# Optimization experiments

Hardware: AMD Instinct MI355X
Metric: run time of the kernel (lower is better)

Reference implementation:

```python
import jax, jax.numpy as jnp
import numpy as np
import math

NEG_INF = -1e29
B, L, H = 16, 1024, 512
D = 2 * H          # feature dim of s and q
GELU_C = math.sqrt(2.0 / math.pi)


def gelu(x):
    return 0.5 * x * (1.0 + jnp.tanh(GELU_C * (x + 0.044715 * x ** 3)))


def mask_softmax(W, m1, m2):
    # joint mask: [B, len1, 1] * [B, 1, len2]
    m = (m1[:, :, None] * m2[:, None, :]).astype(W.dtype)
    return jax.nn.softmax(W + (1.0 - m) * NEG_INF, axis=-1)


def heuristic(x, y, w_r, b_r, w_g, b_g):
    inp = jnp.concatenate([x, y, x * y, x - y], axis=-1)  # [B, L, 8H]
    r = gelu(inp @ w_r.T + b_r)                           # [B, L, 2H]
    g = jax.nn.sigmoid(inp @ w_g.T + b_g)
    return g * r + (1.0 - g) * x


def setup_inputs() -> dict:
    key = jax.random.key(0)
    k = jax.random.split(key, 6)
    s = jax.random.normal(k[0], (B, L, D), jnp.float32)
    q = jax.random.normal(k[1], (B, L, D), jnp.float32)
    s_mask = jnp.ones((B, L), jnp.int32)
    q_mask = jnp.ones((B, L), jnp.int32)
    fan_in = 8 * H
    lim = 1.0 / np.sqrt(fan_in)
    w_r = jax.random.uniform(k[2], (2 * H, fan_in), jnp.float32, -lim, lim)
    b_r = jax.random.uniform(k[3], (2 * H,), jnp.float32, -lim, lim)
    w_g = jax.random.uniform(k[4], (2 * H, fan_in), jnp.float32, -lim, lim)
    b_g = jax.random.uniform(k[5], (2 * H,), jnp.float32, -lim, lim)
    return {"s": s, "q": q, "w_r": w_r, "b_r": b_r, "w_g": w_g, "b_g": b_g,
            "s_mask": s_mask, "q_mask": q_mask}


def reference(s, q, w_r, b_r, w_g, b_g, s_mask, q_mask):
    a = jnp.einsum('bsd,btd->bst', s, q)                  # [B, Ls, Lq]
    b = mask_softmax(a, s_mask, q_mask) @ q               # [B, Ls, D]
    c = mask_softmax(a.swapaxes(-1, -2), q_mask, s_mask) @ s  # [B, Lq, D]
    s_tilde = heuristic(s, b, w_r, b_r, w_g, b_g)
    q_tilde = heuristic(q, c, w_r, b_r, w_g, b_g)
    return (s_tilde, q_tilde)
```

## Files before the change

kernel.cpp:

```cpp
#include <hip/hip_runtime.h>
#include <hip/hip_bf16.h>
#include <math.h>

#define DEVI static __device__ __forceinline__

typedef unsigned short u16;
typedef unsigned int u32;
typedef __bf16 bf16_t;
typedef bf16_t bf16x8 __attribute__((ext_vector_type(8)));
typedef float f32x4 __attribute__((ext_vector_type(4)));

static constexpr int Bb = 16;
static constexpr int L  = 1024;
static constexpr int D  = 1024;
static constexpr int KH = 4096;

DEVI u16 f2bf(float f) {
  union { float f; u32 u; } v; v.f = f;
  u32 r = v.u + 0x7FFFu + ((v.u >> 16) & 1u);
  return (u16)(r >> 16);
}

DEVI float bf2f(u16 b) {
  union { u32 u; float f; } v; v.u = ((u32)b) << 16;
  return v.f;
}

DEVI void gload16(const void* g, void* l) {
  __builtin_amdgcn_global_load_lds((const __attribute__((address_space(1))) u32*)g,
                                   (__attribute__((address_space(3))) u32*)l,
                                   16, 0, 0);
}

DEVI int swz(int row, int col) { return col ^ ((row & 7) << 3); }

__global__ void k_cast_bf16(const float* __restrict__ in, u16* __restrict__ out, int n4) {
  int i = blockIdx.x * blockDim.x + threadIdx.x;
  int stride = gridDim.x * blockDim.x;
  for (; i < n4; i += stride) {
    float4 v = ((const float4*)in)[i];
    ushort4 o;
    o.x = f2bf(v.x); o.y = f2bf(v.y); o.z = f2bf(v.z); o.w = f2bf(v.w);
    ((ushort4*)out)[i] = o;
  }
}

__global__ void k_cast_split(const float* __restrict__ in, u16* __restrict__ hi,
                             u16* __restrict__ lo, int n4) {
  int i = blockIdx.x * blockDim.x + threadIdx.x;
  int stride = gridDim.x * blockDim.x;
  for (; i < n4; i += stride) {
    float4 v = ((const float4*)in)[i];
    ushort4 h, l;
    h.x = f2bf(v.x); h.y = f2bf(v.y); h.z = f2bf(v.z); h.w = f2bf(v.w);
    l.x = f2bf(v.x - bf2f(h.x));
    l.y = f2bf(v.y - bf2f(h.y));
    l.z = f2bf(v.z - bf2f(h.z));
    l.w = f2bf(v.w - bf2f(h.w));
    ((ushort4*)hi)[i] = h;
    ((ushort4*)lo)[i] = l;
  }
}

__global__ void k_feat(const u16* __restrict__ x, const u16* __restrict__ y,
                       u16* __restrict__ xy, u16* __restrict__ xmy, int n8) {
  int i = blockIdx.x * blockDim.x + threadIdx.x;
  int stride = gridDim.x * blockDim.x;
  for (; i < n8; i += stride) {
    bf16x8 xv = ((const bf16x8*)x)[i];
    bf16x8 yv = ((const bf16x8*)y)[i];
    bf16x8 p, d;
    #pragma unroll
    for (int j = 0; j < 8; ++j) {
      float xf = (float)xv[j], yf = (float)yv[j];
      p[j] = (bf16_t)(xf * yf);
      d[j] = (bf16_t)(xf - yf);
    }
    ((bf16x8*)xy)[i] = p;
    ((bf16x8*)xmy)[i] = d;
  }
}

__global__ __launch_bounds__(256)
void k_transpose_bf16(const float* __restrict__ in, u16* __restrict__ out) {
  __shared__ float tile[32][33];
  int b = blockIdx.z;
  int d0 = blockIdx.x * 32;
  int l0 = blockIdx.y * 32;
  const float* ip = in + (size_t)b * L * D;
  u16* op = out + (size_t)b * L * D;
  int tx = threadIdx.x, ty = threadIdx.y;
  #pragma unroll
  for (int j = 0; j < 4; ++j)
    tile[ty + 8 * j][tx] = ip[(size_t)(l0 + ty + 8 * j) * D + d0 + tx];
  __syncthreads();
  #pragma unroll
  for (int j = 0; j < 4; ++j)
    op[(size_t)(d0 + ty + 8 * j) * L + l0 + tx] = f2bf(tile[tx][ty + 8 * j]);
}

template<int OUT_BF16>
__global__ __launch_bounds__(256, 4)
void k_gemm_nt(const u16* __restrict__ A, const u16* __restrict__ Bm, void* __restrict__ Cv,
               int K, int ldc, size_t sA, size_t sB, size_t sC, int tilesN)
{
  __shared__ __align__(16) u16 As[128 * 64];
  __shared__ __align__(16) u16 Bs[128 * 64];
  const int bx = blockIdx.x;
  const int tm = bx / tilesN, tn = bx % tilesN;
  const int b = blockIdx.y;
  const u16* Ap = A + (size_t)b * sA + (size_t)tm * 128 * K;
  const u16* Bp = Bm + (size_t)b * sB + (size_t)tn * 128 * K;
  const int tid = threadIdx.x;
  const int lane = tid & 63, wv = tid >> 6;
  const int wm = wv >> 1, wn = wv & 1;
  const int srow = tid >> 3;
  const int scol = (tid & 7) * 8;
  const int scolswz = swz(srow, scol);
  f32x4 acc[4][4] = {};
  for (int k0 = 0; k0 < K; k0 += 64) {
    #pragma unroll
    for (int i = 0; i < 4; ++i) {
      int row = i * 32 + srow;
      gload16(Ap + (size_t)row * K + k0 + scolswz, &As[row * 64 + scol]);
    }
    #pragma unroll
    for (int i = 0; i < 4; ++i) {
      int row = i * 32 + srow;
      gload16(Bp + (size_t)row * K + k0 + scolswz, &Bs[row * 64 + scol]);
    }
    __syncthreads();
    const int hi8 = (lane >> 4) * 8;
    #pragma unroll
    for (int kk = 0; kk < 64; kk += 32) {
      bf16x8 af[4], bfv[4];
      #pragma unroll
      for (int m = 0; m < 4; ++m) {
        int rr = wm * 64 + m * 16 + (lane & 15);
        af[m] = *(const bf16x8*)&As[rr * 64 + swz(rr, kk + hi8)];
      }
      #pragma unroll
      for (int n = 0; n < 4; ++n) {
        int rr = wn * 64 + n * 16 + (lane & 15);
        bfv[n] = *(const bf16x8*)&Bs[rr * 64 + swz(rr, kk + hi8)];
      }
      #pragma unroll
      for (int m = 0; m < 4; ++m)
        #pragma unroll
        for (int n = 0; n < 4; ++n)
          acc[m][n] = __builtin_amdgcn_mfma_f32_16x16x32_bf16(af[m], bfv[n], acc[m][n], 0, 0, 0);
    }
    __syncthreads();
  }
  const int rb = tm * 128 + wm * 64 + ((lane >> 4) << 2);
  const int cb = tn * 128 + wn * 64 + (lane & 15);
  #pragma unroll
  for (int m = 0; m < 4; ++m)
    #pragma unroll
    for (int n = 0; n < 4; ++n)
      #pragma unroll
      for (int j = 0; j < 4; ++j) {
        int r = rb + m * 16 + j, c = cb + n * 16;
        if (OUT_BF16)
          ((u16*)Cv)[(size_t)b * sC + (size_t)r * ldc + c] = f2bf(acc[m][n][j]);
        else
          ((float*)Cv)[(size_t)b * sC + (size_t)r * ldc + c] = acc[m][n][j];
      }
}

__global__ __launch_bounds__(256, 2)
void k_gemm_nt_split(const u16* __restrict__ Ah, const u16* __restrict__ Al,
                     const u16* __restrict__ Bh, const u16* __restrict__ Bl,
                     float* __restrict__ C, int K, int ldc, size_t sAB, size_t sC, int tilesN)
{
  __shared__ __align__(16) u16 Ahs[128 * 64];
  __shared__ __align__(16) u16 Als[128 * 64];
  __shared__ __align__(16) u16 Bhs[128 * 64];
  __shared__ __align__(16) u16 Bls[128 * 64];
  const int bx = blockIdx.x;
  const int tm = bx / tilesN, tn = bx % tilesN;
  const int b = blockIdx.y;
  const size_t aoff = (size_t)b * sAB + (size_t)tm * 128 * K;
  const size_t boff = (size_t)b * sAB + (size_t)tn * 128 * K;
  const int tid = threadIdx.x;
  const int lane = tid & 63, wv = tid >> 6;
  const int wm = wv >> 1, wn = wv & 1;
  const int srow = tid >> 3;
  const int scol = (tid & 7) * 8;
  const int scolswz = swz(srow, scol);
  f32x4 acc[4][4] = {};
  for (int k0 = 0; k0 < K; k0 += 64) {
    #pragma unroll
    for (int i = 0; i < 4; ++i) {
      int row = i * 32 + srow;
      size_t ga = aoff + (size_t)row * K + k0 + scolswz;
      size_t gb = boff + (size_t)row * K + k0 + scolswz;
      int ls = row * 64 + scol;
      gload16(Ah + ga, &Ahs[ls]);
      gload16(Al + ga, &Als[ls]);
      gload16(Bh + gb, &Bhs[ls]);
      gload16(Bl + gb, &Bls[ls]);
    }
    __syncthreads();
    const int hi8 = (lane >> 4) * 8;
    #pragma unroll
    for (int kk = 0; kk < 64; kk += 32) {
      bf16x8 ah[4], al[4], bh[4], bl[4];
      #pragma unroll
      for (int m = 0; m < 4; ++m) {
        int rr = wm * 64 + m * 16 + (lane & 15);
        int off = rr * 64 + swz(rr, kk + hi8);
        ah[m] = *(const bf16x8*)&Ahs[off];
        al[m] = *(const bf16x8*)&Als[off];
      }
      #pragma unroll
      for (int n = 0; n < 4; ++n) {
        int rr = wn * 64 + n * 16 + (lane & 15);
        int off = rr * 64 + swz(rr, kk + hi8);
        bh[n] = *(const bf16x8*)&Bhs[off];
        bl[n] = *(const bf16x8*)&Bls[off];
      }
      #pragma unroll
      for (int m = 0; m < 4; ++m)
        #pragma unroll
        for (int n = 0; n < 4; ++n) {
          acc[m][n] = __builtin_amdgcn_mfma_f32_16x16x32_bf16(ah[m], bh[n], acc[m][n], 0, 0, 0);
          acc[m][n] = __builtin_amdgcn_mfma_f32_16x16x32_bf16(ah[m], bl[n], acc[m][n], 0, 0, 0);
          acc[m][n] = __builtin_amdgcn_mfma_f32_16x16x32_bf16(al[m], bh[n], acc[m][n], 0, 0, 0);
        }
    }
    __syncthreads();
  }
  const int rb = tm * 128 + wm * 64 + ((lane >> 4) << 2);
  const int cb = tn * 128 + wn * 64 + (lane & 15);
  #pragma unroll
  for (int m = 0; m < 4; ++m)
    #pragma unroll
    for (int n = 0; n < 4; ++n)
      #pragma unroll
      for (int j = 0; j < 4; ++j) {
        int r = rb + m * 16 + j, c = cb + n * 16;
        C[(size_t)b * sC + (size_t)r * ldc + c] = acc[m][n][j];
      }
}

__global__ __launch_bounds__(256)
void k_row_softmax(const float* __restrict__ a, u16* __restrict__ P,
                   const int* __restrict__ m1, const int* __restrict__ m2)
{
  const int row = blockIdx.x, b = blockIdx.y;
  const float* ar = a + ((size_t)b * L + row) * L;
  const int tid = threadIdx.x, lane = tid & 63, wv = tid >> 6;
  __shared__ float redm[4], reds[4];
  float4 v = ((const float4*)ar)[tid];
  int4 mv = ((const int4*)(m2 + (size_t)b * L))[tid];
  const int mr = m1[(size_t)b * L + row];
  float x0 = v.x + (float)(1 - mr * mv.x) * (-1e29f);
  float x1 = v.y + (float)(1 - mr * mv.y) * (-1e29f);
  float x2 = v.z + (float)(1 - mr * mv.z) * (-1e29f);
  float x3 = v.w + (float)(1 - mr * mv.w) * (-1e29f);
  float mx = fmaxf(fmaxf(x0, x1), fmaxf(x2, x3));
  #pragma unroll
  for (int o = 32; o > 0; o >>= 1) mx = fmaxf(mx, __shfl_xor(mx, o));
  if (lane == 0) redm[wv] = mx;
  __syncthreads();
  mx = fmaxf(fmaxf(redm[0], redm[1]), fmaxf(redm[2], redm[3]));
  float e0 = __expf(x0 - mx), e1 = __expf(x1 - mx), e2 = __expf(x2 - mx), e3 = __expf(x3 - mx);
  float s4 = e0 + e1 + e2 + e3;
  #pragma unroll
  for (int o = 32; o > 0; o >>= 1) s4 += __shfl_xor(s4, o);
  if (lane == 0) reds[wv] = s4;
  __syncthreads();
  float inv = 1.0f / (reds[0] + reds[1] + reds[2] + reds[3]);
  ushort4 o;
  o.x = f2bf(e0 * inv); o.y = f2bf(e1 * inv); o.z = f2bf(e2 * inv); o.w = f2bf(e3 * inv);
  ((ushort4*)(P + ((size_t)b * L + row) * L))[tid] = o;
}

__global__ __launch_bounds__(256)
void k_col_softmax(const float* __restrict__ a, u16* __restrict__ P,
                   const int* __restrict__ mrow, const int* __restrict__ mcol)
{
  __shared__ float mred[4][64], lred[4][64];
  __shared__ float Mc[64], Li[64];
  __shared__ u16 T[64][68];
  const int b = blockIdx.y;
  const int c0 = blockIdx.x * 64;
  const int tid = threadIdx.x;
  const int cl = tid & 63;
  const int qr = tid >> 6;
  const int c = c0 + cl;
  const float* ab = a + (size_t)b * L * L;
  const int mc = mcol[(size_t)b * L + c];
  const int* msk = mrow + (size_t)b * L;
  float m = -3.0e38f, l = 0.0f;
  for (int r = qr * 256; r < qr * 256 + 256; ++r) {
    float x = ab[(size_t)r * L + c] + (float)(1 - mc * msk[r]) * (-1e29f);
    float mn = fmaxf(m, x);
    l = l * __expf(m - mn) + __expf(x - mn);
    m = mn;
  }
  mred[qr][cl] = m; lred[qr][cl] = l;
  __syncthreads();
  if (tid < 64) {
    float M = fmaxf(fmaxf(mred[0][tid], mred[1][tid]), fmaxf(mred[2][tid], mred[3][tid]));
    float Lt = lred[0][tid] * __expf(mred[0][tid] - M) + lred[1][tid] * __expf(mred[1][tid] - M)
             + lred[2][tid] * __expf(mred[2][tid] - M) + lred[3][tid] * __expf(mred[3][tid] - M);
    Mc[tid] = M; Li[tid] = 1.0f / Lt;
  }
  __syncthreads();
  const float M = Mc[cl], Linv = Li[cl];
  u16* Pb = P + (size_t)b * L * L;
  const int tl = tid >> 2, sc = (tid & 3) * 16;
  for (int ch = 0; ch < 16; ++ch) {
    #pragma unroll
    for (int rs = 0; rs < 16; ++rs) {
      int r = ch * 64 + qr * 16 + rs;
      float x = ab[(size_t)r * L + c] + (float)(1 - mc * msk[r]) * (-1e29f);
      T[cl][qr * 16 + rs] = f2bf(__expf(x - M) * Linv);
    }
    __syncthreads();
    ushort4* d4 = (ushort4*)(Pb + (size_t)(c0 + tl) * L + ch * 64 + sc);
    #pragma unroll
    for (int jj = 0; jj < 4; ++jj) {
      ushort4 v;
      v.x = T[tl][sc + jj * 4 + 0]; v.y = T[tl][sc + jj * 4 + 1];
      v.z = T[tl][sc + jj * 4 + 2]; v.w = T[tl][sc + jj * 4 + 3];
      d4[jj] = v;
    }
    __syncthreads();
  }
}

__global__ __launch_bounds__(512, 2)
void k_heur3(const u16* __restrict__ X, const u16* __restrict__ Y,
             const u16* __restrict__ XY, const u16* __restrict__ XMY,
             const u16* __restrict__ Wr, const u16* __restrict__ Wg,
             const float* __restrict__ br, const float* __restrict__ bg,
             const float* __restrict__ Xf, float* __restrict__ out)
{
  __shared__ __align__(16) u16 As[2][256 * 64];
  __shared__ __align__(16) u16 Wrs[2][128 * 64];
  __shared__ __align__(16) u16 Wgs[2][128 * 64];
  const int bx = blockIdx.x;
  const int xcd = bx & 7, li = bx >> 3;
  const int tn = li & 7, tm = xcd * 8 + (li >> 3);
  const size_t rowBase = (size_t)tm * 256;
  const int tid = threadIdx.x, lane = tid & 63;
  const int wv = tid >> 6;
  const int wm = wv >> 1, wn = wv & 1;
  const int srow = tid >> 3;
  const int scol = (tid & 7) * 8;
  const int scolswz = swz(srow, scol);
  f32x4 accR[4][4] = {}, accG[4][4] = {};

  auto stage = [&](int t, int buf) {
    const int fa = t >> 4;
    const u16* ap = (fa == 0) ? X : (fa == 1) ? Y : (fa == 2) ? XY : XMY;
    const int kcol = (t & 15) * 64;
    #pragma unroll
    for (int i = 0; i < 4; ++i) {
      int row = i * 64 + srow;
      gload16(ap + (rowBase + row) * (size_t)D + kcol + scolswz, &As[buf][row * 64 + scol]);
    }
    const size_t wcol = (size_t)t * 64;
    #pragma unroll
    for (int i = 0; i < 2; ++i) {
      int row = i * 64 + srow;
      size_t woff = ((size_t)tn * 128 + row) * (size_t)KH + wcol + scolswz;
      gload16(Wr + woff, &Wrs[buf][row * 64 + scol]);
      gload16(Wg + woff, &Wgs[buf][row * 64 + scol]);
    }
  };

  stage(0, 0);
  __syncthreads();

  for (int t = 0; t < 64; ++t) {
    const int cur = t & 1;
    if (t < 63) stage(t + 1, cur ^ 1);

    const int hi8 = (lane >> 4) * 8;
    #pragma unroll
    for (int kk = 0; kk < 64; kk += 32) {
      bf16x8 af[4];
      #pragma unroll
      for (int m = 0; m < 4; ++m) {
        int rr = wm * 64 + m * 16 + (lane & 15);
        af[m] = *(const bf16x8*)&As[cur][rr * 64 + swz(rr, kk + hi8)];
      }
      #pragma unroll
      for (int n = 0; n < 4; ++n) {
        int rr = wn * 64 + n * 16 + (lane & 15);
        int off = rr * 64 + swz(rr, kk + hi8);
        bf16x8 bR = *(const bf16x8*)&Wrs[cur][off];
        bf16x8 bG = *(const bf16x8*)&Wgs[cur][off];
        #pragma unroll
        for (int m = 0; m < 4; ++m) {
          accR[m][n] = __builtin_amdgcn_mfma_f32_16x16x32_bf16(af[m], bR, accR[m][n], 0, 0, 0);
          accG[m][n] = __builtin_amdgcn_mfma_f32_16x16x32_bf16(af[m], bG, accG[m][n], 0, 0, 0);
        }
      }
    }
    __syncthreads();
  }

  const int rb = wm * 64 + ((lane >> 4) << 2);
  const int cb = tn * 128 + wn * 64 + (lane & 15);
  #pragma unroll
  for (int m = 0; m < 4; ++m)
    #pragma unroll
    for (int n = 0; n < 4; ++n)
      #pragma unroll
      for (int j = 0; j < 4; ++j) {
        size_t row = rowBase + rb + m * 16 + j;
        int col = cb + n * 16;
        float r = accR[m][n][j] + br[col];
        float g = accG[m][n][j] + bg[col];
        float th = tanhf(0.79788456080286535588f * (r + 0.044715f * r * r * r));
        float gl = 0.5f * r * (1.0f + th);
        float sg = 1.0f / (1.0f + __expf(-g));
        float xv = Xf[row * (size_t)D + col];
        out[row * (size_t)D + col] = sg * gl + (1.0f - sg) * xv;
      }
}

extern "C" void kernel_launch(void* const* d_in, const int* in_sizes, int n_in,
                              void* d_out, int out_size, void* d_ws, size_t ws_size,
                              hipStream_t stream)
{
  (void)in_sizes; (void)n_in; (void)out_size; (void)ws_size;
  const float* s    = (const float*)d_in[0];
  const float* q    = (const float*)d_in[1];
  const float* w_r  = (const float*)d_in[2];
  const float* b_r  = (const float*)d_in[3];
  const float* w_g  = (const float*)d_in[4];
  const float* b_g  = (const float*)d_in[5];
  const int* s_mask = (const int*)d_in[6];
  const int* q_mask = (const int*)d_in[7];
  float* out = (float*)d_out;

  const size_t SQ = (size_t)Bb * L * D;
  const size_t W  = (size_t)D * KH;
  const size_t S1 = (size_t)L * D;

  char* p = (char*)d_ws;
  u16* s_bf  = (u16*)p; p += SQ * 2;
  u16* q_bf  = (u16*)p; p += SQ * 2;
  u16* buf1  = (u16*)p; p += SQ * 2;
  u16* buf2  = (u16*)p; p += SQ * 2;
  u16* b_bf  = (u16*)p; p += SQ * 2;
  u16* c_bf  = (u16*)p; p += SQ * 2;
  u16* wr_bf = (u16*)p; p += W * 2;
  u16* wg_bf = (u16*)p; p += W * 2;

  float* a  = out;
  u16*   P1 = (u16*)(out + SQ);
  u16*   P2 = (u16*)(out + SQ + SQ / 2);

  dim3 blk(256);
  k_cast_split<<<4096, blk, 0, stream>>>(s, s_bf, buf1, (int)(SQ / 4));
  k_cast_split<<<4096, blk, 0, stream>>>(q, q_bf, buf2, (int)(SQ / 4));
  k_cast_bf16<<<2048, blk, 0, stream>>>(w_r, wr_bf, (int)(W / 4));
  k_cast_bf16<<<2048, blk, 0, stream>>>(w_g, wg_bf, (int)(W / 4));

  dim3 ggrid(64, Bb);
  k_gemm_nt_split<<<ggrid, blk, 0, stream>>>(s_bf, buf1, q_bf, buf2, a, D, L, S1, (size_t)L * L, 8);
  k_row_softmax<<<dim3(L, Bb), blk, 0, stream>>>(a, P1, s_mask, q_mask);
  k_col_softmax<<<dim3(L / 64, Bb), blk, 0, stream>>>(a, P2, s_mask, q_mask);

  dim3 tgrid(D / 32, L / 32, Bb), tblk(32, 8);
  k_transpose_bf16<<<tgrid, tblk, 0, stream>>>(s, buf1);
  k_transpose_bf16<<<tgrid, tblk, 0, stream>>>(q, buf2);

  k_gemm_nt<1><<<ggrid, blk, 0, stream>>>(P1, buf2, b_bf, L, D, (size_t)L * L, S1, S1, 8);
  k_gemm_nt<1><<<ggrid, blk, 0, stream>>>(P2, buf1, c_bf, L, D, (size_t)L * L, S1, S1, 8);

  k_feat<<<2048, blk, 0, stream>>>(s_bf, b_bf, buf1, buf2, (int)(SQ / 8));
  k_heur3<<<512, dim3(512), 0, stream>>>(s_bf, b_bf, buf1, buf2, wr_bf, wg_bf, b_r, b_g, s, out);

  k_feat<<<2048, blk, 0, stream>>>(q_bf, c_bf, buf1, buf2, (int)(SQ / 8));
  k_heur3<<<512, dim3(512), 0, stream>>>(q_bf, c_bf, buf1, buf2, wr_bf, wg_bf, b_r, b_g, q, out + SQ);
}
```

Measured before the change: 1.042 ms.

## Interleave Wr/Wg rows into one weight matrix and use a single-accumulator heuristic GEMM

Weights w_r and w_g are cast into one interleaved bf16 matrix (alternating rows), so the heuristic GEMM becomes a single 2048-column GEMM with one accumulator set. The r and g values are paired afterwards with a lane shuffle in the epilogue. The new kernel uses 128x128 tiles, 256 threads and 4 blocks per CU, with a single LDS buffer instead of double-buffered staging. Smaller tiles give more blocks and lower register pressure, but prefetch overlap is lost, half the lanes do redundant epilogue work, and the smaller tiles mean less data reuse.

```diff
diff --git a/kernel.cpp b/kernel.cpp
--- a/kernel.cpp
+++ b/kernel.cpp
@@ -33,17 +33,6 @@
 }
 
 DEVI int swz(int row, int col) { return col ^ ((row & 7) << 3); }
-
-__global__ void k_cast_bf16(const float* __restrict__ in, u16* __restrict__ out, int n4) {
-  int i = blockIdx.x * blockDim.x + threadIdx.x;
-  int stride = gridDim.x * blockDim.x;
-  for (; i < n4; i += stride) {
-    float4 v = ((const float4*)in)[i];
-    ushort4 o;
-    o.x = f2bf(v.x); o.y = f2bf(v.y); o.z = f2bf(v.z); o.w = f2bf(v.w);
-    ((ushort4*)out)[i] = o;
-  }
-}
 
 __global__ void k_cast_split(const float* __restrict__ in, u16* __restrict__ hi,
                              u16* __restrict__ lo, int n4) {
@@ -59,6 +48,21 @@
     l.w = f2bf(v.w - bf2f(h.w));
     ((ushort4*)hi)[i] = h;
     ((ushort4*)lo)[i] = l;
+  }
+}
+
+__global__ void k_wcat(const float* __restrict__ wr, const float* __restrict__ wg,
+                       u16* __restrict__ wcat, int n4) {
+  int i = blockIdx.x * blockDim.x + threadIdx.x;
+  int stride = gridDim.x * blockDim.x;
+  for (; i < n4; i += stride) {
+    int j = i >> 10;
+    int c4 = i & 1023;
+    const float* src = ((j & 1) ? wg : wr) + (size_t)(j >> 1) * 4096 + c4 * 4;
+    float4 v = *(const float4*)src;
+    ushort4 o;
+    o.x = f2bf(v.x); o.y = f2bf(v.y); o.z = f2bf(v.z); o.w = f2bf(v.w);
+    ((ushort4*)wcat)[i] = o;
   }
 }
 
@@ -332,97 +336,89 @@
   }
 }
 
-__global__ __launch_bounds__(512, 2)
-void k_heur3(const u16* __restrict__ X, const u16* __restrict__ Y,
+__global__ __launch_bounds__(256, 4)
+void k_heur5(const u16* __restrict__ X, const u16* __restrict__ Y,
              const u16* __restrict__ XY, const u16* __restrict__ XMY,
-             const u16* __restrict__ Wr, const u16* __restrict__ Wg,
+             const u16* __restrict__ Wc,
              const float* __restrict__ br, const float* __restrict__ bg,
              const float* __restrict__ Xf, float* __restrict__ out)
 {
-  __shared__ __align__(16) u16 As[2][256 * 64];
-  __shared__ __align__(16) u16 Wrs[2][128 * 64];
-  __shared__ __align__(16) u16 Wgs[2][128 * 64];
+  __shared__ __align__(16) u16 As[128 * 64];
+  __shared__ __align__(16) u16 Bs[128 * 64];
   const int bx = blockIdx.x;
   const int xcd = bx & 7, li = bx >> 3;
-  const int tn = li & 7, tm = xcd * 8 + (li >> 3);
-  const size_t rowBase = (size_t)tm * 256;
-  const int tid = threadIdx.x, lane = tid & 63;
-  const int wv = tid >> 6;
+  const int tn = li & 15, tm = xcd * 16 + (li >> 4);
+  const size_t rowBase = (size_t)tm * 128;
+  const int colBase = tn * 128;
+  const u16* Bp = Wc + (size_t)colBase * KH;
+  const int tid = threadIdx.x;
+  const int lane = tid & 63, wv = tid >> 6;
   const int wm = wv >> 1, wn = wv & 1;
   const int srow = tid >> 3;
   const int scol = (tid & 7) * 8;
   const int scolswz = swz(srow, scol);
-  f32x4 accR[4][4] = {}, accG[4][4] = {};
-
-  auto stage = [&](int t, int buf) {
-    const int fa = t >> 4;
-    const u16* ap = (fa == 0) ? X : (fa == 1) ? Y : (fa == 2) ? XY : XMY;
-    const int kcol = (t & 15) * 64;
+  f32x4 acc[4][4] = {};
+  for (int k0 = 0; k0 < KH; k0 += 64) {
+    const u16* ap = (k0 < 2048) ? (k0 < 1024 ? X : Y) : (k0 < 3072 ? XY : XMY);
+    const int kc = k0 & 1023;
     #pragma unroll
     for (int i = 0; i < 4; ++i) {
-      int row = i * 64 + srow;
-      gload16(ap + (rowBase + row) * (size_t)D + kcol + scolswz, &As[buf][row * 64 + scol]);
-    }
-    const size_t wcol = (size_t)t * 64;
-    #pragma unroll
-    for (int i = 0; i < 2; ++i) {
-      int row = i * 64 + srow;
-      size_t woff = ((size_t)tn * 128 + row) * (size_t)KH + wcol + scolswz;
-      gload16(Wr + woff, &Wrs[buf][row * 64 + scol]);
-      gload16(Wg + woff, &Wgs[buf][row * 64 + scol]);
-    }
-  };
-
-  stage(0, 0);
-  __syncthreads();
-
-  for (int t = 0; t < 64; ++t) {
-    const int cur = t & 1;
-    if (t < 63) stage(t + 1, cur ^ 1);
-
+      int row = i * 32 + srow;
+      gload16(ap + (rowBase + row) * (size_t)D + kc + scolswz, &As[row * 64 + scol]);
+    }
+    #pragma unroll
+    for (int i = 0; i < 4; ++i) {
+      int row = i * 32 + srow;
+      gload16(Bp + (size_t)row * KH + k0 + scolswz, &Bs[row * 64 + scol]);
+    }
+    __syncthreads();
     const int hi8 = (lane >> 4) * 8;
     #pragma unroll
     for (int kk = 0; kk < 64; kk += 32) {
-      bf16x8 af[4];
+      bf16x8 af[4], bfv[4];
       #pragma unroll
       for (int m = 0; m < 4; ++m) {
         int rr = wm * 64 + m * 16 + (lane & 15);
-        af[m] = *(const bf16x8*)&As[cur][rr * 64 + swz(rr, kk + hi8)];
+        af[m] = *(const bf16x8*)&As[rr * 64 + swz(rr, kk + hi8)];
       }
       #pragma unroll
       for (int n = 0; n < 4; ++n) {
         int rr = wn * 64 + n * 16 + (lane & 15);
-        int off = rr * 64 + swz(rr, kk + hi8);
-        bf16x8 bR = *(const bf16x8*)&Wrs[cur][off];
-        bf16x8 bG = *(const bf16x8*)&Wgs[cur][off];
+        bfv[n] = *(const bf16x8*)&Bs[rr * 64 + swz(rr, kk + hi8)];
+      }
+      #pragma unroll
+      for (int m = 0; m < 4; ++m)
         #pragma unroll
-        for (int m = 0; m < 4; ++m) {
-          accR[m][n] = __builtin_amdgcn_mfma_f32_16x16x32_bf16(af[m], bR, accR[m][n], 0, 0, 0);
-          accG[m][n] = __builtin_amdgcn_mfma_f32_16x16x32_bf16(af[m], bG, accG[m][n], 0, 0, 0);
-        }
-      }
-    }
-    __syncthreads();
-  }
-
+        for (int n = 0; n < 4; ++n)
+          acc[m][n] = __builtin_amdgcn_mfma_f32_16x16x32_bf16(af[m], bfv[n], acc[m][n], 0, 0, 0);
+    }
+    __syncthreads();
+  }
   const int rb = wm * 64 + ((lane >> 4) << 2);
-  const int cb = tn * 128 + wn * 64 + (lane & 15);
+  const int cbl = wn * 64 + (lane & 15);
+  const int odd = lane & 1;
   #pragma unroll
   for (int m = 0; m < 4; ++m)
     #pragma unroll
-    for (int n = 0; n < 4; ++n)
+    for (int n = 0; n < 4; ++n) {
+      int ncol = colBase + cbl + n * 16;
+      int cc = ncol >> 1;
       #pragma unroll
       for (int j = 0; j < 4; ++j) {
         size_t row = rowBase + rb + m * 16 + j;
-        int col = cb + n * 16;
-        float r = accR[m][n][j] + br[col];
-        float g = accG[m][n][j] + bg[col];
+        float v = acc[m][n][j];
+        float pv = __shfl_xor(v, 1);
+        float r = odd ? pv : v;
+        float g = odd ? v : pv;
+        r += br[cc]; g += bg[cc];
         float th = tanhf(0.79788456080286535588f * (r + 0.044715f * r * r * r));
         float gl = 0.5f * r * (1.0f + th);
         float sg = 1.0f / (1.0f + __expf(-g));
-        float xv = Xf[row * (size_t)D + col];
-        out[row * (size_t)D + col] = sg * gl + (1.0f - sg) * xv;
-      }
+        float xv = Xf[row * (size_t)D + cc];
+        float res = sg * gl + (1.0f - sg) * xv;
+        if (!odd) out[row * (size_t)D + cc] = res;
+      }
+    }
 }
 
 extern "C" void kernel_launch(void* const* d_in, const int* in_sizes, int n_in,
@@ -451,8 +447,7 @@
   u16* buf2  = (u16*)p; p += SQ * 2;
   u16* b_bf  = (u16*)p; p += SQ * 2;
   u16* c_bf  = (u16*)p; p += SQ * 2;
-  u16* wr_bf = (u16*)p; p += W * 2;
-  u16* wg_bf = (u16*)p; p += W * 2;
+  u16* wcat  = (u16*)p; p += 2 * W * 2;
 
   float* a  = out;
   u16*   P1 = (u16*)(out + SQ);
@@ -461,8 +456,7 @@
   dim3 blk(256);
   k_cast_split<<<4096, blk, 0, stream>>>(s, s_bf, buf1, (int)(SQ / 4));
   k_cast_split<<<4096, blk, 0, stream>>>(q, q_bf, buf2, (int)(SQ / 4));
-  k_cast_bf16<<<2048, blk, 0, stream>>>(w_r, wr_bf, (int)(W / 4));
-  k_cast_bf16<<<2048, blk, 0, stream>>>(w_g, wg_bf, (int)(W / 4));
+  k_wcat<<<4096, blk, 0, stream>>>(w_r, w_g, wcat, (int)(2 * W / 4));
 
   dim3 ggrid(64, Bb);
   k_gemm_nt_split<<<ggrid, blk, 0, stream>>>(s_bf, buf1, q_bf, buf2, a, D, L, S1, (size_t)L * L, 8);
@@ -477,8 +471,8 @@
   k_gemm_nt<1><<<ggrid, blk, 0, stream>>>(P2, buf1, c_bf, L, D, (size_t)L * L, S1, S1, 8);
 
   k_feat<<<2048, blk, 0, stream>>>(s_bf, b_bf, buf1, buf2, (int)(SQ / 8));
-  k_heur3<<<512, dim3(512), 0, stream>>>(s_bf, b_bf, buf1, buf2, wr_bf, wg_bf, b_r, b_g, s, out);
+  k_heur5<<<2048, blk, 0, stream>>>(s_bf, b_bf, buf1, buf2, wcat, b_r, b_g, s, out);
 
   k_feat<<<2048, blk, 0, stream>>>(q_bf, c_bf, buf1, buf2, (int)(SQ / 8));
-  k_heur3<<<512, dim3(512), 0, stream>>>(q_bf, c_bf, buf1, buf2, wr_bf, wg_bf, b_r, b_g, q, out + SQ);
-}
+  k_heur5<<<2048, blk, 0, stream>>>(q_bf, c_bf, buf1, buf2, wcat, b_r, b_g, q, out + SQ);
+}
```

Measured after the change: 1.062 ms. No clear change (+1.9%).
